# Kernel tuning notes

Hardware: AMD Instinct MI355X
Metric: run time of the kernel (lower is better)

The kernel has to match this reference:

```python
import jax, jax.numpy as jnp
import numpy as np

NPIX = 256
NCHAN = 1
NVIS = 50000
CELL_ARCSEC = 0.005                      # GridCoords cell_size [arcsec]
ARCSEC = np.float32(np.pi / 180.0 / 3600.0)  # arcsec -> radians


def setup_inputs() -> dict:
    key = jax.random.key(0)
    k1, k2, k3 = jax.random.split(key, 3)
    # BaseCube learned parameter (pre-softplus)
    base_cube = 0.05 * jax.random.normal(k1, (NCHAN, NPIX, NPIX), dtype=jnp.float32)
    # Nyquist limit in kilolambda set by the pixel size
    max_kl = 1.0 / (2.0 * CELL_ARCSEC * float(ARCSEC)) / 1e3
    uu = (jax.random.uniform(k2, (NVIS,), dtype=jnp.float32) - 0.5) * max_kl
    vv = (jax.random.uniform(k3, (NVIS,), dtype=jnp.float32) - 0.5) * max_kl
    return {"base_cube": base_cube, "uu": uu, "vv": vv}


def _forward(base_cube, uu, vv):
    # --- BaseCube: softplus pixel mapping to enforce positivity ---
    img = jax.nn.softplus(base_cube)                       # (C, Y, X)
    # --- HannConvCube: fixed 3x3 Hann kernel, per channel, zero pad ---
    h = jnp.array([0.25, 0.5, 0.25], dtype=img.dtype)
    kern = jnp.outer(h, h)[None, None]                     # (1, 1, 3, 3)
    img = jax.lax.conv_general_dilated(img[:, None], kern, (1, 1), 'SAME')[:, 0]
    # --- ImageCube(passthrough=True): identity ---
    # --- NuFFT: exact type-2 non-uniform DFT, separable in u/v ---
    cell_rad = jnp.float32(CELL_ARCSEC) * ARCSEC
    coords = (jnp.arange(NPIX, dtype=jnp.float32) - NPIX // 2) * cell_rad  # sky coords [rad]
    u_lam = uu * 1e3   # kilolambda -> lambda
    v_lam = vv * 1e3
    # phase matrices: (K, X) and (K, Y)
    a = jnp.exp(-2j * jnp.pi * (u_lam[:, None] * coords[None, :])).astype(jnp.complex64)
    b = jnp.exp(-2j * jnp.pi * (v_lam[:, None] * coords[None, :])).astype(jnp.complex64)
    # t[c,k,y] = sum_x img[c,y,x] a[k,x]  -> (C, K, Y)
    t = jnp.einsum('cyx,kx->cky', img.astype(jnp.complex64), a)
    # vis[c,k] = sum_y t[c,k,y] b[k,y], scaled by pixel solid angle
    vis = jnp.einsum('cky,ky->ck', t, b) * (cell_rad * cell_rad)
    return vis  # (C, K) complex64 model visibilities


def reference(base_cube, uu, vv):
    return _forward(base_cube, uu, vv)
```

## Files before the change

kernel.cpp:

```cpp
#include <hip/hip_runtime.h>
#include <hip/hip_bf16.h>
#include <math.h>

#define NPIX 256
#define HALF 128
#define NVIS 50000
#define BLK  256
#define NKPAD 50176
#define NBLK_VIS (NKPAD / 64)
#define TWO_PI_F 6.28318530717958647692f

typedef __attribute__((ext_vector_type(8))) short short8;
typedef __attribute__((ext_vector_type(4))) float float4v;

__device__ __forceinline__ float cell_rad_f() {
    const float arcsec = (float)(M_PI / 180.0 / 3600.0);
    return 0.005f * arcsec;
}

__device__ __forceinline__ unsigned pack_bf2(float lo, float hi) {
    __hip_bfloat162 h = __float22bfloat162_rn(make_float2(lo, hi));
    return *reinterpret_cast<unsigned*>(&h);
}

#define SPR 18
#define SPC 130
__global__ __launch_bounds__(BLK) void prep_kernel(const float* __restrict__ base,
                                                   unsigned short* __restrict__ wimg) {
    __shared__ float sp[SPR][SPC];
    const int yt = blockIdx.x >> 1, xh = blockIdx.x & 1;
    const int y0 = yt * 16, x0 = xh * 128;
    const int tid = threadIdx.x;

    for (int idx = tid; idx < SPR * SPC; idx += BLK) {
        int r = idx / SPC, c = idx - r * SPC;
        int y = y0 - 1 + r, x = x0 - 1 + c;
        float v = 0.f;
        if ((unsigned)y < NPIX && (unsigned)x < NPIX)
            v = log1pf(expf(base[y * NPIX + x]));
        sp[r][c] = v;
    }
    __syncthreads();

    {
        int yl = tid >> 4, oc = tid & 15;
        union { unsigned short u[8]; uint4 v; } pk;
        #pragma unroll
        for (int e = 0; e < 8; ++e) {
            int cl = oc * 8 + e;
            float top = sp[yl    ][cl] + 2.f * sp[yl    ][cl + 1] + sp[yl    ][cl + 2];
            float mid = sp[yl + 1][cl] + 2.f * sp[yl + 1][cl + 1] + sp[yl + 1][cl + 2];
            float bot = sp[yl + 2][cl] + 2.f * sp[yl + 2][cl + 1] + sp[yl + 2][cl + 2];
            float cv  = 0.0625f * (top + 2.f * mid + bot);
            __hip_bfloat16 h = __float2bfloat16(cv);
            pk.u[e] = *reinterpret_cast<unsigned short*>(&h);
        }
        int o = xh * 16 + oc;
        int s = o >> 2, g = o & 3;
        size_t off = (((size_t)yt * 8 + s) * 64 + g * 16 + yl) * 8;
        *(uint4*)(wimg + off) = pk.v;
    }
}

__global__ __launch_bounds__(BLK) void vis_mfma(const float* __restrict__ uu,
                                                const float* __restrict__ vv,
                                                const unsigned short* __restrict__ wimg,
                                                float* __restrict__ out) {
    __shared__ uint4 lds4[2048];
    unsigned short* lds = (unsigned short*)lds4;

    const int tid  = threadIdx.x;
    const int wid  = tid >> 6, lane = tid & 63;
    const int lo   = lane & 15, hi = lane >> 4;
    const int k0   = blockIdx.x * 64 + wid * 16;

    const float cell = cell_rad_f();
    const float sc   = TWO_PI_F * 1e3f * cell;

    int ka = k0 + lo; if (ka > NVIS - 1) ka = NVIS - 1;
    const float del = sc * uu[ka];
    float cd, sd; sincosf(del, &sd, &cd);
    union AB { short8 v; unsigned u[4]; };
    AB Are[8], Aim[8];
    #pragma unroll
    for (int s = 0; s < 8; ++s) {
        float th0 = del * (float)(s * 32 + hi * 8 - HALF);
        float s0, c0; sincosf(th0, &s0, &c0);
        float ar = c0, ai = -s0;
        #pragma unroll
        for (int ep = 0; ep < 4; ++ep) {
            float ar0 = ar, ai0 = ai;
            float ar1 = fmaf(ar0, cd,  ai0 * sd);
            float ai1 = fmaf(ai0, cd, -ar0 * sd);
            Are[s].u[ep] = pack_bf2(ar0, ar1);
            Aim[s].u[ep] = pack_bf2(ai0, ai1);
            ar = fmaf(ar1, cd,  ai1 * sd);
            ai = fmaf(ai1, cd, -ar1 * sd);
        }
    }

    float br[4], bi[4], str[4], sts[4], eps;
    #pragma unroll
    for (int r = 0; r < 4; ++r) {
        int kk = k0 + hi * 4 + r; if (kk > NVIS - 1) kk = NVIS - 1;
        eps = sc * vv[kk];
        float w0 = eps * (float)(lo - HALF);
        float sw, cw; sincosf(w0, &sw, &cw);
        br[r] = cw; bi[r] = -sw;
        float s16, c16; sincosf(eps * 16.f, &s16, &c16);
        str[r] = c16; sts[r] = s16;
    }

    float visr[4] = {0.f, 0.f, 0.f, 0.f}, visi[4] = {0.f, 0.f, 0.f, 0.f};

    for (int p = 0; p < 4; ++p) {
        __syncthreads();
        const uint4* src = (const uint4*)wimg + (size_t)p * 2048;
        #pragma unroll
        for (int i = 0; i < 8; ++i) lds4[i * BLK + tid] = src[i * BLK + tid];
        __syncthreads();

        #pragma unroll
        for (int ytl = 0; ytl < 4; ++ytl) {
            float4v accR = {0.f, 0.f, 0.f, 0.f}, accI = {0.f, 0.f, 0.f, 0.f};
            #pragma unroll
            for (int s = 0; s < 8; ++s) {
                short8 B = *(const short8*)&lds[(((ytl * 8 + s) * 64) + lane) * 8];
                accR = __builtin_amdgcn_mfma_f32_16x16x32_bf16(Are[s].v, B, accR, 0, 0, 0);
                accI = __builtin_amdgcn_mfma_f32_16x16x32_bf16(Aim[s].v, B, accI, 0, 0, 0);
            }
            #pragma unroll
            for (int r = 0; r < 4; ++r) {
                visr[r] = fmaf(accR[r], br[r], visr[r]); visr[r] = fmaf(-accI[r], bi[r], visr[r]);
                visi[r] = fmaf(accI[r], br[r], visi[r]); visi[r] = fmaf( accR[r], bi[r], visi[r]);
                float nbr = fmaf(br[r], str[r],  bi[r] * sts[r]);
                float nbi = fmaf(bi[r], str[r], -br[r] * sts[r]);
                br[r] = nbr; bi[r] = nbi;
            }
        }
    }

    #pragma unroll
    for (int r = 0; r < 4; ++r) {
        #pragma unroll
        for (int d = 1; d < 16; d <<= 1) {
            visr[r] += __shfl_xor(visr[r], d);
            visi[r] += __shfl_xor(visi[r], d);
        }
    }
    if (lo == 0) {
        const float c2 = cell * cell;
        #pragma unroll
        for (int r = 0; r < 4; ++r) {
            int kk = k0 + hi * 4 + r;
            if (kk < NVIS) {
                out[kk]        = visr[r] * c2;
                out[NVIS + kk] = visi[r] * c2;
            }
        }
    }
}

extern "C" void kernel_launch(void* const* d_in, const int* in_sizes, int n_in,
                              void* d_out, int out_size, void* d_ws, size_t ws_size,
                              hipStream_t stream) {
    const float* base = (const float*)d_in[0];
    const float* uu   = (const float*)d_in[1];
    const float* vv   = (const float*)d_in[2];
    (void)in_sizes; (void)n_in; (void)out_size; (void)ws_size;

    unsigned short* wimg = (unsigned short*)d_ws;

    prep_kernel<<<32, BLK, 0, stream>>>(base, wimg);
    vis_mfma<<<NBLK_VIS, BLK, 0, stream>>>(uu, vv, wimg, (float*)d_out);
}
```

Before: 88.91 us.

## Switch visibility DFT to 32x32x16 MFMA with image as A operand

Replaces the 16x16x32 bf16 MFMA tiling with 32x32x16 MFMA: each wave now handles 32 visibilities, with the image tile as the A operand and per-visibility u-phase vectors as B. The prep kernel writes the blurred image in a matching layout. The v-phase is applied with a rotation recurrence built from powers of exp(-i*eps), and the final reduction becomes a single cross-half shuffle instead of a 16-lane butterfly. Blocks shrink to 128 threads and each thread holds 16 phase fragments, which raises register pressure. The longer phase recurrences may also cost some accuracy.

```diff
diff --git a/kernel.cpp b/kernel.cpp
--- a/kernel.cpp
+++ b/kernel.cpp
@@ -5,13 +5,14 @@
 #define NPIX 256
 #define HALF 128
 #define NVIS 50000
-#define BLK  256
-#define NKPAD 50176
-#define NBLK_VIS (NKPAD / 64)
 #define TWO_PI_F 6.28318530717958647692f
 
-typedef __attribute__((ext_vector_type(8))) short short8;
-typedef __attribute__((ext_vector_type(4))) float float4v;
+#define VBLK 128
+#define KPB  64
+#define NBLK_VIS ((NVIS + KPB - 1) / KPB)
+
+typedef __attribute__((ext_vector_type(8)))  short short8;
+typedef __attribute__((ext_vector_type(16))) float f32x16;
 
 __device__ __forceinline__ float cell_rad_f() {
     const float arcsec = (float)(M_PI / 180.0 / 3600.0);
@@ -25,14 +26,14 @@
 
 #define SPR 18
 #define SPC 130
-__global__ __launch_bounds__(BLK) void prep_kernel(const float* __restrict__ base,
+__global__ __launch_bounds__(256) void prep_kernel(const float* __restrict__ base,
                                                    unsigned short* __restrict__ wimg) {
     __shared__ float sp[SPR][SPC];
-    const int yt = blockIdx.x >> 1, xh = blockIdx.x & 1;
-    const int y0 = yt * 16, x0 = xh * 128;
+    const int by = blockIdx.x >> 1, xh = blockIdx.x & 1;
+    const int y0 = by * 16, x0 = xh * 128;
     const int tid = threadIdx.x;
 
-    for (int idx = tid; idx < SPR * SPC; idx += BLK) {
+    for (int idx = tid; idx < SPR * SPC; idx += 256) {
         int r = idx / SPC, c = idx - r * SPC;
         int y = y0 - 1 + r, x = x0 - 1 + c;
         float v = 0.f;
@@ -55,108 +56,117 @@
             __hip_bfloat16 h = __float2bfloat16(cv);
             pk.u[e] = *reinterpret_cast<unsigned short*>(&h);
         }
-        int o = xh * 16 + oc;
-        int s = o >> 2, g = o & 3;
-        size_t off = (((size_t)yt * 8 + s) * 64 + g * 16 + yl) * 8;
+        int gx   = x0 + oc * 8;
+        int step = gx >> 4, hv = (gx >> 3) & 1;
+        int y    = y0 + yl;
+        int yt   = y >> 5, ycol = y & 31;
+        size_t off = (((size_t)yt * 16 + step) * 64 + hv * 32 + ycol) * 8;
         *(uint4*)(wimg + off) = pk.v;
     }
 }
 
-__global__ __launch_bounds__(BLK) void vis_mfma(const float* __restrict__ uu,
-                                                const float* __restrict__ vv,
-                                                const unsigned short* __restrict__ wimg,
-                                                float* __restrict__ out) {
+__global__ __launch_bounds__(VBLK) void vis_mfma(const float* __restrict__ uu,
+                                                 const float* __restrict__ vv,
+                                                 const unsigned short* __restrict__ wimg,
+                                                 float* __restrict__ out) {
     __shared__ uint4 lds4[2048];
     unsigned short* lds = (unsigned short*)lds4;
 
     const int tid  = threadIdx.x;
     const int wid  = tid >> 6, lane = tid & 63;
-    const int lo   = lane & 15, hi = lane >> 4;
-    const int k0   = blockIdx.x * 64 + wid * 16;
+    const int kcol = lane & 31, hv = lane >> 5;
+    const int k0   = blockIdx.x * KPB + wid * 32;
 
     const float cell = cell_rad_f();
     const float sc   = TWO_PI_F * 1e3f * cell;
 
-    int ka = k0 + lo; if (ka > NVIS - 1) ka = NVIS - 1;
+    int ka = k0 + kcol; if (ka > NVIS - 1) ka = NVIS - 1;
     const float del = sc * uu[ka];
+    const float eps = sc * vv[ka];
+
     float cd, sd; sincosf(del, &sd, &cd);
-    union AB { short8 v; unsigned u[4]; };
-    AB Are[8], Aim[8];
+    float c16, s16; sincosf(16.f * del, &s16, &c16);
+    float th0 = del * (float)(hv * 8 - HALF);
+    float s0, c0; sincosf(th0, &s0, &c0);
+    float bar = c0, bai = -s0;
+
+    union BF { short8 v; unsigned u[4]; };
+    BF Bre[16], Bim[16];
     #pragma unroll
-    for (int s = 0; s < 8; ++s) {
-        float th0 = del * (float)(s * 32 + hi * 8 - HALF);
-        float s0, c0; sincosf(th0, &s0, &c0);
-        float ar = c0, ai = -s0;
+    for (int step = 0; step < 16; ++step) {
+        float ar = bar, ai = bai;
         #pragma unroll
         for (int ep = 0; ep < 4; ++ep) {
-            float ar0 = ar, ai0 = ai;
-            float ar1 = fmaf(ar0, cd,  ai0 * sd);
-            float ai1 = fmaf(ai0, cd, -ar0 * sd);
-            Are[s].u[ep] = pack_bf2(ar0, ar1);
-            Aim[s].u[ep] = pack_bf2(ai0, ai1);
+            float ar1 = fmaf(ar, cd,  ai * sd);
+            float ai1 = fmaf(ai, cd, -ar * sd);
+            Bre[step].u[ep] = pack_bf2(ar, ar1);
+            Bim[step].u[ep] = pack_bf2(ai, ai1);
             ar = fmaf(ar1, cd,  ai1 * sd);
             ai = fmaf(ai1, cd, -ar1 * sd);
         }
+        float nbr = fmaf(bar, c16,  bai * s16);
+        float nbi = fmaf(bai, c16, -bar * s16);
+        bar = nbr; bai = nbi;
     }
 
-    float br[4], bi[4], str[4], sts[4], eps;
-    #pragma unroll
-    for (int r = 0; r < 4; ++r) {
-        int kk = k0 + hi * 4 + r; if (kk > NVIS - 1) kk = NVIS - 1;
-        eps = sc * vv[kk];
-        float w0 = eps * (float)(lo - HALF);
-        float sw, cw; sincosf(w0, &sw, &cw);
-        br[r] = cw; bi[r] = -sw;
-        float s16, c16; sincosf(eps * 16.f, &s16, &c16);
-        str[r] = c16; sts[r] = s16;
-    }
+    float ce, se; sincosf(eps, &se, &ce);
+    const float r1r = ce, r1i = -se;
+    float r2r = fmaf(r1r, r1r, -r1i * r1i), r2i = 2.f * r1r * r1i;
+    float r4r = fmaf(r2r, r2r, -r2i * r2i), r4i = 2.f * r2r * r2i;
+    float r8r = fmaf(r4r, r4r, -r4i * r4i), r8i = 2.f * r4r * r4i;
 
-    float visr[4] = {0.f, 0.f, 0.f, 0.f}, visi[4] = {0.f, 0.f, 0.f, 0.f};
+    float visr = 0.f, visi = 0.f;
 
     for (int p = 0; p < 4; ++p) {
         __syncthreads();
         const uint4* src = (const uint4*)wimg + (size_t)p * 2048;
         #pragma unroll
-        for (int i = 0; i < 8; ++i) lds4[i * BLK + tid] = src[i * BLK + tid];
+        for (int i = 0; i < 16; ++i) lds4[i * VBLK + tid] = src[i * VBLK + tid];
         __syncthreads();
 
         #pragma unroll
-        for (int ytl = 0; ytl < 4; ++ytl) {
-            float4v accR = {0.f, 0.f, 0.f, 0.f}, accI = {0.f, 0.f, 0.f, 0.f};
+        for (int t = 0; t < 2; ++t) {
+            f32x16 aR = {0.f}, aI = {0.f};
             #pragma unroll
-            for (int s = 0; s < 8; ++s) {
-                short8 B = *(const short8*)&lds[(((ytl * 8 + s) * 64) + lane) * 8];
-                accR = __builtin_amdgcn_mfma_f32_16x16x32_bf16(Are[s].v, B, accR, 0, 0, 0);
-                accI = __builtin_amdgcn_mfma_f32_16x16x32_bf16(Aim[s].v, B, accI, 0, 0, 0);
+            for (int i = 1; i < 16; ++i) { aR[i] = 0.f; aI[i] = 0.f; }
+            #pragma unroll
+            for (int step = 0; step < 16; ++step) {
+                short8 A = *(const short8*)&lds[(((t * 16 + step) * 64) + lane) * 8];
+                aR = __builtin_amdgcn_mfma_f32_32x32x16_bf16(A, Bre[step].v, aR, 0, 0, 0);
+                aI = __builtin_amdgcn_mfma_f32_32x32x16_bf16(A, Bim[step].v, aI, 0, 0, 0);
             }
+            const int Y0 = (p * 2 + t) * 32;
+            float w0 = eps * (float)(Y0 + 4 * hv - HALF);
+            float sw, cw; sincosf(w0, &sw, &cw);
+            float bgr = cw, bgi = -sw;
             #pragma unroll
-            for (int r = 0; r < 4; ++r) {
-                visr[r] = fmaf(accR[r], br[r], visr[r]); visr[r] = fmaf(-accI[r], bi[r], visr[r]);
-                visi[r] = fmaf(accI[r], br[r], visi[r]); visi[r] = fmaf( accR[r], bi[r], visi[r]);
-                float nbr = fmaf(br[r], str[r],  bi[r] * sts[r]);
-                float nbi = fmaf(bi[r], str[r], -br[r] * sts[r]);
-                br[r] = nbr; bi[r] = nbi;
+            for (int grp = 0; grp < 4; ++grp) {
+                float br_ = bgr, bi_ = bgi;
+                #pragma unroll
+                for (int j = 0; j < 4; ++j) {
+                    int r = grp * 4 + j;
+                    visr = fmaf(aR[r], br_, visr); visr = fmaf(-aI[r], bi_, visr);
+                    visi = fmaf(aI[r], br_, visi); visi = fmaf( aR[r], bi_, visi);
+                    float nr = fmaf(br_, r1r, -bi_ * r1i);
+                    float ni = fmaf(bi_, r1r,  br_ * r1i);
+                    br_ = nr; bi_ = ni;
+                }
+                float ngr = fmaf(bgr, r8r, -bgi * r8i);
+                float ngi = fmaf(bgi, r8r,  bgr * r8i);
+                bgr = ngr; bgi = ngi;
             }
         }
     }
 
-    #pragma unroll
-    for (int r = 0; r < 4; ++r) {
-        #pragma unroll
-        for (int d = 1; d < 16; d <<= 1) {
-            visr[r] += __shfl_xor(visr[r], d);
-            visi[r] += __shfl_xor(visi[r], d);
-        }
-    }
-    if (lo == 0) {
-        const float c2 = cell * cell;
-        #pragma unroll
-        for (int r = 0; r < 4; ++r) {
-            int kk = k0 + hi * 4 + r;
-            if (kk < NVIS) {
-                out[kk]        = visr[r] * c2;
-                out[NVIS + kk] = visi[r] * c2;
-            }
+    visr += __shfl_xor(visr, 32);
+    visi += __shfl_xor(visi, 32);
+
+    if (hv == 0) {
+        int kk = k0 + kcol;
+        if (kk < NVIS) {
+            const float c2 = cell * cell;
+            out[kk]        = visr * c2;
+            out[NVIS + kk] = visi * c2;
         }
     }
 }
@@ -171,6 +181,6 @@
 
     unsigned short* wimg = (unsigned short*)d_ws;
 
-    prep_kernel<<<32, BLK, 0, stream>>>(base, wimg);
-    vis_mfma<<<NBLK_VIS, BLK, 0, stream>>>(uu, vv, wimg, (float*)d_out);
+    prep_kernel<<<32, 256, 0, stream>>>(base, wimg);
+    vis_mfma<<<NBLK_VIS, VBLK, 0, stream>>>(uu, vv, wimg, (float*)d_out);
 }
```

New measurement: 108.4 us. +21.9%, slower.
